# Optimization experiments

Hardware: AMD Instinct MI355X
Metric: run time of the kernel (lower is better)

## Reference

```python
import jax, jax.numpy as jnp
import numpy as np

NODES = 1024   # LSTM hidden size (nodes)
LAYERS = 5     # LSTM layers
SEQ = 2048     # sequence length
B = 1          # batch (hardcoded by init_hidden in the torch module)
IN_DIM = 30    # 12 + 12 + 6 concatenated features
OUT_DIM = 12   # n_input_state_real
SLOPE = 0.01   # F.leaky_relu default negative slope


def setup_inputs() -> dict:
    key = jax.random.key(0)
    ks = jax.random.split(key, 8)
    s = 0.02
    return dict(
        sim=jax.random.normal(ks[0], (B, SEQ, 12), dtype=jnp.float32),
        real=jax.random.normal(ks[1], (B, SEQ, 12), dtype=jnp.float32),
        act=jax.random.normal(ks[2], (B, SEQ, 6), dtype=jnp.float32),
        W1=jax.random.normal(ks[3], (NODES, IN_DIM), dtype=jnp.float32) * s,
        b1=jnp.zeros((NODES,), dtype=jnp.float32),
        # all LSTM layers have input size NODES (nn.LSTM(nodes, nodes, layers))
        W_ih=jax.random.normal(ks[4], (LAYERS, 4 * NODES, NODES), dtype=jnp.float32) * s,
        W_hh=jax.random.normal(ks[5], (LAYERS, 4 * NODES, NODES), dtype=jnp.float32) * s,
        b_ih=jnp.zeros((LAYERS, 4 * NODES), dtype=jnp.float32),
        b_hh=jnp.zeros((LAYERS, 4 * NODES), dtype=jnp.float32),
        W2=jax.random.normal(ks[6], (OUT_DIM, NODES), dtype=jnp.float32) * s,
        b2=jnp.zeros((OUT_DIM,), dtype=jnp.float32),
        h0=jnp.zeros((LAYERS, B, NODES), dtype=jnp.float32),
        c0=jnp.zeros((LAYERS, B, NODES), dtype=jnp.float32),
    )


def _lstm_layer(x, h0, c0, W_ih, W_hh, b_ih, b_hh):
    # x: [T, B, N]. Precompute input projection for all timesteps (big GEMM),
    # then scan the recurrence. PyTorch gate order: i, f, g, o.
    x_proj = jnp.einsum('tbn,gn->tbg', x, W_ih) + b_ih  # [T, B, 4N]

    def step(carry, xp):
        h, c = carry
        gates = xp + h @ W_hh.T + b_hh
        i, f, g, o = jnp.split(gates, 4, axis=-1)
        c = jax.nn.sigmoid(f) * c + jax.nn.sigmoid(i) * jnp.tanh(g)
        h = jax.nn.sigmoid(o) * jnp.tanh(c)
        return (h, c), h

    _, ys = jax.lax.scan(step, (h0, c0), x_proj)
    return ys  # [T, B, N]


def reference(sim, real, act, W1, b1, W_ih, W_hh, b_ih, b_hh, W2, b2, h0, c0):
    x = jnp.concatenate((sim, real, act), axis=2)      # [B, T, 30]
    x = jax.nn.leaky_relu(x @ W1.T + b1, SLOPE)        # [B, T, N]
    x = x.transpose(1, 0, 2)                           # [T, B, N] (time-major)
    for l in range(LAYERS):
        x = _lstm_layer(x, h0[l], c0[l], W_ih[l], W_hh[l], b_ih[l], b_hh[l])
    x = jax.nn.leaky_relu(x.transpose(1, 0, 2), SLOPE)  # [B, T, N]
    return x @ W2.T + b2                                # [B, T, 12]
```

## Files before the change

### kernel.cpp

```cpp
#include <hip/hip_runtime.h>

#define NODES 1024
#define LAYERS 5
#define SEQ 2048
#define IN_DIM 30
#define OUT_DIM 12
#define SLOPE 0.01f
#define RING_D 16

typedef unsigned long long u64;

__device__ __forceinline__ float sigmoidf_(float x) { return 1.0f / (1.0f + expf(-x)); }

__global__ __launch_bounds__(256) void fc1_kernel(
    const float* __restrict__ sim, const float* __restrict__ realv,
    const float* __restrict__ act, const float* __restrict__ W1,
    const float* __restrict__ b1, float* __restrict__ x_out)
{
    int t = blockIdx.x;
    __shared__ float in_s[IN_DIM];
    int tid = threadIdx.x;
    if (tid < 12) in_s[tid] = sim[t * 12 + tid];
    else if (tid < 24) in_s[tid] = realv[t * 12 + (tid - 12)];
    else if (tid < 30) in_s[tid] = act[t * 6 + (tid - 24)];
    __syncthreads();
    for (int n = tid; n < NODES; n += 256) {
        float acc = b1[n];
        const float* w = W1 + n * IN_DIM;
        #pragma unroll
        for (int k = 0; k < IN_DIM; ++k) acc += w[k] * in_s[k];
        x_out[t * NODES + n] = acc > 0.f ? acc : SLOPE * acc;
    }
}

#define BM 64
#define BN 64
#define BK 16

__global__ __launch_bounds__(256) void xproj_kernel(
    const float* __restrict__ X, const float* __restrict__ W,
    const float* __restrict__ bih, const float* __restrict__ bhh,
    float* __restrict__ XP)
{
    const int GN = 4 * NODES;
    int bm = blockIdx.y;
    int bn = blockIdx.x;
    __shared__ float As[BK][BM];
    __shared__ float Bs[BK][BN];
    int tid = threadIdx.x;
    int tx = tid % 16, ty = tid / 16;
    int arow = tid / 4;
    int acol4 = (tid % 4) * 4;
    float acc[4][4] = {};

    for (int k0 = 0; k0 < NODES; k0 += BK) {
        float4 a = *(const float4*)&X[(size_t)(bm * BM + arow) * NODES + k0 + acol4];
        As[acol4 + 0][arow] = a.x; As[acol4 + 1][arow] = a.y;
        As[acol4 + 2][arow] = a.z; As[acol4 + 3][arow] = a.w;
        float4 b = *(const float4*)&W[(size_t)(bn * BN + arow) * NODES + k0 + acol4];
        Bs[acol4 + 0][arow] = b.x; Bs[acol4 + 1][arow] = b.y;
        Bs[acol4 + 2][arow] = b.z; Bs[acol4 + 3][arow] = b.w;
        __syncthreads();
        #pragma unroll
        for (int k = 0; k < BK; ++k) {
            float ra[4], rb[4];
            #pragma unroll
            for (int m = 0; m < 4; ++m) ra[m] = As[k][ty * 4 + m];
            #pragma unroll
            for (int n = 0; n < 4; ++n) rb[n] = Bs[k][tx * 4 + n];
            #pragma unroll
            for (int m = 0; m < 4; ++m)
                #pragma unroll
                for (int n = 0; n < 4; ++n)
                    acc[m][n] += ra[m] * rb[n];
        }
        __syncthreads();
    }
    #pragma unroll
    for (int m = 0; m < 4; ++m) {
        int t = bm * BM + ty * 4 + m;
        int g0 = bn * BN + tx * 4;
        float4 o;
        o.x = acc[m][0] + bih[g0 + 0] + bhh[g0 + 0];
        o.y = acc[m][1] + bih[g0 + 1] + bhh[g0 + 1];
        o.z = acc[m][2] + bih[g0 + 2] + bhh[g0 + 2];
        o.w = acc[m][3] + bih[g0 + 3] + bhh[g0 + 3];
        *(float4*)&XP[(size_t)t * GN + g0] = o;
    }
}

__global__ __launch_bounds__(512, 2)
void lstm_group_kernel(
    const float* __restrict__ Wih,
    const float* __restrict__ Whh,
    const float* __restrict__ bih,
    const float* __restrict__ bhh,
    const float* __restrict__ XP,
    const float* __restrict__ h0,
    const float* __restrict__ c0,
    float* __restrict__ Yout,
    u64* rings, int l_base, int NL)
{
    __shared__ u64 mir[3][2][16][64];

    const int tid = threadIdx.x;
    const int wave = tid >> 6, lane = tid & 63;
    const int lg = wave >> 2;
    const int q = wave & 3;
    const int j = blockIdx.x * 4 + q;
    const int l = l_base + lg;
    const bool first = (lg == 0);
    const bool last  = (lg == NL - 1);

    float whh[4][16];
    {
        const float* wp = Whh + (size_t)l * 4 * NODES * NODES;
        #pragma unroll
        for (int g = 0; g < 4; ++g)
            #pragma unroll
            for (int k = 0; k < 16; ++k)
                whh[g][k] = wp[(size_t)(g * NODES + j) * NODES + lane + k * 64];
    }
    float wih[4][16];
    if (!first) {
        const float* wp = Wih + (size_t)l * 4 * NODES * NODES;
        #pragma unroll
        for (int g = 0; g < 4; ++g)
            #pragma unroll
            for (int k = 0; k < 16; ++k)
                wih[g][k] = wp[(size_t)(g * NODES + j) * NODES + lane + k * 64];
    }
    float bg[4] = {0.f, 0.f, 0.f, 0.f};
    if (!first) {
        #pragma unroll
        for (int g = 0; g < 4; ++g)
            bg[g] = bih[l * 4 * NODES + g * NODES + j] + bhh[l * 4 * NODES + g * NODES + j];
    }

    for (int idx = tid; idx < 3 * 2 * 16 * 64; idx += blockDim.x)
        ((u64*)mir)[idx] = 0;

    u64* ring_own  = rings + (size_t)l * RING_D * NODES;
    u64* ring_prev = rings + (size_t)(l > 0 ? l - 1 : 0) * RING_D * NODES;
    u64* ring_next = rings + (size_t)(!last ? l + 1 : l) * RING_D * NODES;

    float c = c0[l * NODES + j];
    float xpg[4] = {0.f, 0.f, 0.f, 0.f};
    if (first) {
        #pragma unroll
        for (int g = 0; g < 4; ++g) xpg[g] = XP[(size_t)0 * 4 * NODES + g * NODES + j];
    }
    __syncthreads();

    for (int t = 0; t < SEQ; ++t) {
        u64 thr = 0;
        u64* tp = ring_next + (size_t)((t + 2) % RING_D) * NODES + j;
        const bool do_thr = (!last) && (t >= RING_D);
        if (do_thr && lane == 0)
            thr = __hip_atomic_load(tp, __ATOMIC_RELAXED, __HIP_MEMORY_SCOPE_AGENT);

        float gate[4] = {0.f, 0.f, 0.f, 0.f};

        if (t == 0) {
            #pragma unroll
            for (int k = 0; k < 16; ++k) {
                float hh = h0[l * NODES + lane + k * 64];
                #pragma unroll
                for (int g = 0; g < 4; ++g) gate[g] += whh[g][k] * hh;
            }
        } else {
            u64* so = ring_own + (size_t)(t % RING_D) * NODES;
            const int mid = lg;
            const int par = t & 1;
            u64 mybuf[4];
            for (;;) {
                #pragma unroll
                for (int kk = 0; kk < 4; ++kk)
                    mybuf[kk] = __hip_atomic_load(&so[lane + (q * 4 + kk) * 64],
                                                  __ATOMIC_RELAXED, __HIP_MEMORY_SCOPE_AGENT);
                bool ok = true;
                #pragma unroll
                for (int kk = 0; kk < 4; ++kk) ok = ok && ((int)(mybuf[kk] >> 32) == t);
                if (ok) break;
            }
            #pragma unroll
            for (int kk = 0; kk < 4; ++kk)
                __hip_atomic_store(&mir[mid][par][q * 4 + kk][lane], mybuf[kk],
                                   __ATOMIC_RELAXED, __HIP_MEMORY_SCOPE_WORKGROUP);
            u64 vo[16];
            for (;;) {
                bool ok = true;
                #pragma unroll
                for (int k = 0; k < 16; ++k) {
                    vo[k] = __hip_atomic_load(&mir[mid][par][k][lane],
                                              __ATOMIC_RELAXED, __HIP_MEMORY_SCOPE_WORKGROUP);
                    ok = ok && ((int)(vo[k] >> 32) == t);
                }
                if (ok) break;
            }
            #pragma unroll
            for (int k = 0; k < 16; ++k) {
                float hh = __uint_as_float((unsigned)vo[k]);
                #pragma unroll
                for (int g = 0; g < 4; ++g) gate[g] += whh[g][k] * hh;
            }
        }

        if (!first) {
            u64* si = ring_prev + (size_t)((t + 1) % RING_D) * NODES;
            const int par = (t + 1) & 1;
            u64 mybuf[4];
            for (;;) {
                #pragma unroll
                for (int kk = 0; kk < 4; ++kk)
                    mybuf[kk] = __hip_atomic_load(&si[lane + (q * 4 + kk) * 64],
                                                  __ATOMIC_RELAXED, __HIP_MEMORY_SCOPE_AGENT);
                bool ok = true;
                #pragma unroll
                for (int kk = 0; kk < 4; ++kk) ok = ok && ((int)(mybuf[kk] >> 32) == t + 1);
                if (ok) break;
            }
            #pragma unroll
            for (int kk = 0; kk < 4; ++kk)
                __hip_atomic_store(&mir[2][par][q * 4 + kk][lane], mybuf[kk],
                                   __ATOMIC_RELAXED, __HIP_MEMORY_SCOPE_WORKGROUP);
            u64 vi[16];
            for (;;) {
                bool ok = true;
                #pragma unroll
                for (int k = 0; k < 16; ++k) {
                    vi[k] = __hip_atomic_load(&mir[2][par][k][lane],
                                              __ATOMIC_RELAXED, __HIP_MEMORY_SCOPE_WORKGROUP);
                    ok = ok && ((int)(vi[k] >> 32) == t + 1);
                }
                if (ok) break;
            }
            #pragma unroll
            for (int k = 0; k < 16; ++k) {
                float xx = __uint_as_float((unsigned)vi[k]);
                #pragma unroll
                for (int g = 0; g < 4; ++g) gate[g] += wih[g][k] * xx;
            }
        }

        #pragma unroll
        for (int g = 0; g < 4; ++g) {
            float acc = gate[g];
            #pragma unroll
            for (int off = 32; off > 0; off >>= 1) acc += __shfl_xor(acc, off);
            gate[g] = acc + (first ? xpg[g] : bg[g]);
        }

        float ig = sigmoidf_(gate[0]);
        float fg = sigmoidf_(gate[1]);
        float gg = tanhf(gate[2]);
        float og = sigmoidf_(gate[3]);
        c = fg * c + ig * gg;
        float h = og * tanhf(c);

        if (lane == 0) {
            if (do_thr) {
                int thresh = t + 2 - RING_D;
                u64 tv = thr;
                while ((int)(tv >> 32) < thresh)
                    tv = __hip_atomic_load(tp, __ATOMIC_RELAXED, __HIP_MEMORY_SCOPE_AGENT);
            }
            u64 pv = ((u64)(unsigned)(t + 1) << 32) | (u64)__float_as_uint(h);
            __hip_atomic_store(&ring_own[(size_t)((t + 1) % RING_D) * NODES + j], pv,
                               __ATOMIC_RELAXED, __HIP_MEMORY_SCOPE_AGENT);
            if (last) Yout[(size_t)t * NODES + j] = h;
        }

        if (first && t + 1 < SEQ) {
            #pragma unroll
            for (int g = 0; g < 4; ++g)
                xpg[g] = XP[(size_t)(t + 1) * 4 * NODES + g * NODES + j];
        }
    }
}

__global__ __launch_bounds__(256) void fc2_kernel(
    const float* __restrict__ Y, const float* __restrict__ W2,
    const float* __restrict__ b2, float* __restrict__ out)
{
    int t = blockIdx.x;
    __shared__ float ys[NODES];
    int tid = threadIdx.x;
    for (int n = tid; n < NODES; n += 256) {
        float v = Y[(size_t)t * NODES + n];
        ys[n] = v > 0.f ? v : SLOPE * v;
    }
    __syncthreads();
    int wave = tid >> 6, lane = tid & 63;
    for (int o = wave; o < OUT_DIM; o += 4) {
        float acc = 0.f;
        const float* w = W2 + o * NODES;
        #pragma unroll
        for (int k = 0; k < 16; ++k) acc += w[lane + k * 64] * ys[lane + k * 64];
        #pragma unroll
        for (int off = 32; off > 0; off >>= 1) acc += __shfl_xor(acc, off);
        if (lane == 0) out[t * OUT_DIM + o] = acc + b2[o];
    }
}

extern "C" void kernel_launch(void* const* d_in, const int* in_sizes, int n_in,
                              void* d_out, int out_size, void* d_ws, size_t ws_size,
                              hipStream_t stream) {
    const float* sim  = (const float*)d_in[0];
    const float* relv = (const float*)d_in[1];
    const float* act  = (const float*)d_in[2];
    const float* W1   = (const float*)d_in[3];
    const float* b1   = (const float*)d_in[4];
    const float* W_ih = (const float*)d_in[5];
    const float* W_hh = (const float*)d_in[6];
    const float* b_ih = (const float*)d_in[7];
    const float* b_hh = (const float*)d_in[8];
    const float* W2   = (const float*)d_in[9];
    const float* b2   = (const float*)d_in[10];
    const float* h0   = (const float*)d_in[11];
    const float* c0   = (const float*)d_in[12];
    float* out = (float*)d_out;

    char* ws = (char*)d_ws;
    float* xbuf = (float*)ws;
    float* xp   = (float*)(ws + (size_t)8 * 1024 * 1024);
    float* ya   = (float*)(ws + (size_t)40 * 1024 * 1024);
    u64*   rings = (u64*)(ws + (size_t)48 * 1024 * 1024);

    hipMemsetAsync(rings, 0, (size_t)LAYERS * RING_D * NODES * sizeof(u64), stream);

    fc1_kernel<<<SEQ, 256, 0, stream>>>(sim, relv, act, W1, b1, xbuf);

    xproj_kernel<<<dim3(4 * NODES / BN, SEQ / BM), 256, 0, stream>>>(
        xbuf, W_ih, b_ih, b_hh, xp);
    {
        int l_base = 0, nl = 2;
        void* args[] = { (void*)&W_ih, (void*)&W_hh, (void*)&b_ih, (void*)&b_hh,
                         (void*)&xp, (void*)&h0, (void*)&c0, (void*)&ya,
                         (void*)&rings, (void*)&l_base, (void*)&nl };
        hipLaunchCooperativeKernel((const void*)lstm_group_kernel,
                                   dim3(256), dim3(512), args, 0, stream);
    }

    xproj_kernel<<<dim3(4 * NODES / BN, SEQ / BM), 256, 0, stream>>>(
        ya, W_ih + (size_t)2 * 4 * NODES * NODES,
        b_ih + 2 * 4 * NODES, b_hh + 2 * 4 * NODES, xp);
    {
        int l_base = 2, nl = 2;
        void* args[] = { (void*)&W_ih, (void*)&W_hh, (void*)&b_ih, (void*)&b_hh,
                         (void*)&xp, (void*)&h0, (void*)&c0, (void*)&ya,
                         (void*)&rings, (void*)&l_base, (void*)&nl };
        hipLaunchCooperativeKernel((const void*)lstm_group_kernel,
                                   dim3(256), dim3(512), args, 0, stream);
    }

    xproj_kernel<<<dim3(4 * NODES / BN, SEQ / BM), 256, 0, stream>>>(
        ya, W_ih + (size_t)4 * 4 * NODES * NODES,
        b_ih + 4 * 4 * NODES, b_hh + 4 * 4 * NODES, xp);
    {
        int l_base = 4, nl = 1;
        void* args[] = { (void*)&W_ih, (void*)&W_hh, (void*)&b_ih, (void*)&b_hh,
                         (void*)&xp, (void*)&h0, (void*)&c0, (void*)&xbuf,
                         (void*)&rings, (void*)&l_base, (void*)&nl };
        hipLaunchCooperativeKernel((const void*)lstm_group_kernel,
                                   dim3(256), dim3(256), args, 0, stream);
    }

    fc2_kernel<<<SEQ, 256, 0, stream>>>(xbuf, W2, b2, out);
}
```

Before: 32.87 ms.

## Share layer outputs through LDS mirror instead of re-reading previous layer's ring

Within a workgroup that hosts two consecutive layers, the next layer now reads its input h directly from the producing layer's shared-memory mirror rather than polling the previous layer's global ring and copying it into a separate mirror. The global back-pressure check on the next layer's ring is replaced by an LDS-based check that the consumer has advanced before the mirror slot is overwritten, plus a final publish after the loop. This removes one global polling pass per step and shrinks LDS, but couples the producer's progress to the consumer's within the block and relies on correct parity and threshold handling.

```diff
diff --git a/kernel.cpp b/kernel.cpp
--- a/kernel.cpp
+++ b/kernel.cpp
@@ -101,7 +101,7 @@
     float* __restrict__ Yout,
     u64* rings, int l_base, int NL)
 {
-    __shared__ u64 mir[3][2][16][64];
+    __shared__ u64 mir[2][2][16][64];
 
     const int tid = threadIdx.x;
     const int wave = tid >> 6, lane = tid & 63;
@@ -137,12 +137,10 @@
             bg[g] = bih[l * 4 * NODES + g * NODES + j] + bhh[l * 4 * NODES + g * NODES + j];
     }
 
-    for (int idx = tid; idx < 3 * 2 * 16 * 64; idx += blockDim.x)
+    for (int idx = tid; idx < 2 * 2 * 16 * 64; idx += blockDim.x)
         ((u64*)mir)[idx] = 0;
 
-    u64* ring_own  = rings + (size_t)l * RING_D * NODES;
-    u64* ring_prev = rings + (size_t)(l > 0 ? l - 1 : 0) * RING_D * NODES;
-    u64* ring_next = rings + (size_t)(!last ? l + 1 : l) * RING_D * NODES;
+    u64* ring_own = rings + (size_t)l * RING_D * NODES;
 
     float c = c0[l * NODES + j];
     float xpg[4] = {0.f, 0.f, 0.f, 0.f};
@@ -153,12 +151,6 @@
     __syncthreads();
 
     for (int t = 0; t < SEQ; ++t) {
-        u64 thr = 0;
-        u64* tp = ring_next + (size_t)((t + 2) % RING_D) * NODES + j;
-        const bool do_thr = (!last) && (t >= RING_D);
-        if (do_thr && lane == 0)
-            thr = __hip_atomic_load(tp, __ATOMIC_RELAXED, __HIP_MEMORY_SCOPE_AGENT);
-
         float gate[4] = {0.f, 0.f, 0.f, 0.f};
 
         if (t == 0) {
@@ -170,7 +162,6 @@
             }
         } else {
             u64* so = ring_own + (size_t)(t % RING_D) * NODES;
-            const int mid = lg;
             const int par = t & 1;
             u64 mybuf[4];
             for (;;) {
@@ -183,16 +174,29 @@
                 for (int kk = 0; kk < 4; ++kk) ok = ok && ((int)(mybuf[kk] >> 32) == t);
                 if (ok) break;
             }
+            if (!last && t >= 2) {
+                const int thresh = t - 2;
+                for (;;) {
+                    bool ok = true;
+                    #pragma unroll
+                    for (int qq = 0; qq < 4; ++qq) {
+                        u64 v = __hip_atomic_load(&mir[lg + 1][par][qq * 4][lane],
+                                                  __ATOMIC_RELAXED, __HIP_MEMORY_SCOPE_WORKGROUP);
+                        ok = ok && ((int)(v >> 32) >= thresh);
+                    }
+                    if (ok) break;
+                }
+            }
             #pragma unroll
             for (int kk = 0; kk < 4; ++kk)
-                __hip_atomic_store(&mir[mid][par][q * 4 + kk][lane], mybuf[kk],
+                __hip_atomic_store(&mir[lg][par][q * 4 + kk][lane], mybuf[kk],
                                    __ATOMIC_RELAXED, __HIP_MEMORY_SCOPE_WORKGROUP);
             u64 vo[16];
             for (;;) {
                 bool ok = true;
                 #pragma unroll
                 for (int k = 0; k < 16; ++k) {
-                    vo[k] = __hip_atomic_load(&mir[mid][par][k][lane],
+                    vo[k] = __hip_atomic_load(&mir[lg][par][k][lane],
                                               __ATOMIC_RELAXED, __HIP_MEMORY_SCOPE_WORKGROUP);
                     ok = ok && ((int)(vo[k] >> 32) == t);
                 }
@@ -207,29 +211,13 @@
         }
 
         if (!first) {
-            u64* si = ring_prev + (size_t)((t + 1) % RING_D) * NODES;
             const int par = (t + 1) & 1;
-            u64 mybuf[4];
-            for (;;) {
-                #pragma unroll
-                for (int kk = 0; kk < 4; ++kk)
-                    mybuf[kk] = __hip_atomic_load(&si[lane + (q * 4 + kk) * 64],
-                                                  __ATOMIC_RELAXED, __HIP_MEMORY_SCOPE_AGENT);
-                bool ok = true;
-                #pragma unroll
-                for (int kk = 0; kk < 4; ++kk) ok = ok && ((int)(mybuf[kk] >> 32) == t + 1);
-                if (ok) break;
-            }
-            #pragma unroll
-            for (int kk = 0; kk < 4; ++kk)
-                __hip_atomic_store(&mir[2][par][q * 4 + kk][lane], mybuf[kk],
-                                   __ATOMIC_RELAXED, __HIP_MEMORY_SCOPE_WORKGROUP);
             u64 vi[16];
             for (;;) {
                 bool ok = true;
                 #pragma unroll
                 for (int k = 0; k < 16; ++k) {
-                    vi[k] = __hip_atomic_load(&mir[2][par][k][lane],
+                    vi[k] = __hip_atomic_load(&mir[lg - 1][par][k][lane],
                                               __ATOMIC_RELAXED, __HIP_MEMORY_SCOPE_WORKGROUP);
                     ok = ok && ((int)(vi[k] >> 32) == t + 1);
                 }
@@ -259,12 +247,6 @@
         float h = og * tanhf(c);
 
         if (lane == 0) {
-            if (do_thr) {
-                int thresh = t + 2 - RING_D;
-                u64 tv = thr;
-                while ((int)(tv >> 32) < thresh)
-                    tv = __hip_atomic_load(tp, __ATOMIC_RELAXED, __HIP_MEMORY_SCOPE_AGENT);
-            }
             u64 pv = ((u64)(unsigned)(t + 1) << 32) | (u64)__float_as_uint(h);
             __hip_atomic_store(&ring_own[(size_t)((t + 1) % RING_D) * NODES + j], pv,
                                __ATOMIC_RELAXED, __HIP_MEMORY_SCOPE_AGENT);
@@ -276,6 +258,37 @@
             for (int g = 0; g < 4; ++g)
                 xpg[g] = XP[(size_t)(t + 1) * 4 * NODES + g * NODES + j];
         }
+    }
+
+    if (!last) {
+        const int par = SEQ & 1;
+        const int thresh = SEQ - 2;
+        for (;;) {
+            bool ok = true;
+            #pragma unroll
+            for (int qq = 0; qq < 4; ++qq) {
+                u64 v = __hip_atomic_load(&mir[lg + 1][par][qq * 4][lane],
+                                          __ATOMIC_RELAXED, __HIP_MEMORY_SCOPE_WORKGROUP);
+                ok = ok && ((int)(v >> 32) >= thresh);
+            }
+            if (ok) break;
+        }
+        u64* so = ring_own + (size_t)(SEQ % RING_D) * NODES;
+        u64 mybuf[4];
+        for (;;) {
+            #pragma unroll
+            for (int kk = 0; kk < 4; ++kk)
+                mybuf[kk] = __hip_atomic_load(&so[lane + (q * 4 + kk) * 64],
+                                              __ATOMIC_RELAXED, __HIP_MEMORY_SCOPE_AGENT);
+            bool ok = true;
+            #pragma unroll
+            for (int kk = 0; kk < 4; ++kk) ok = ok && ((int)(mybuf[kk] >> 32) == SEQ);
+            if (ok) break;
+        }
+        #pragma unroll
+        for (int kk = 0; kk < 4; ++kk)
+            __hip_atomic_store(&mir[lg][par][q * 4 + kk][lane], mybuf[kk],
+                               __ATOMIC_RELAXED, __HIP_MEMORY_SCOPE_WORKGROUP);
     }
 }
 
```

New measurement: 26.33 ms. 1.25x faster.
